# Kernel optimization log

Measured on AMD Instinct MI355X. Metric: run time of the kernel, lower is better.

## Reference

```python
import jax, jax.numpy as jnp
import numpy as np
import math

H = 12          # num_attention_heads
DIM = 768       # hidden_size
HD = DIM // H   # attention_head_size
B = 8           # batch
S = 1024        # max_seqlen
NNZ = B * S     # total_nnz (all sequences full length)


def setup_inputs() -> dict:
    key = jax.random.key(0)
    k1, k2, k3, k4 = jax.random.split(key, 4)
    hidden_states = jax.random.normal(k1, (NNZ, DIM), jnp.float32)
    cu_seqlens = jnp.arange(B + 1, dtype=jnp.int32) * S
    indices = jnp.arange(NNZ, dtype=jnp.int32)
    attn_mask = jnp.ones((B, S), jnp.int32)
    bias = jax.random.normal(k2, (B, H, S, S), jnp.float32) * 0.1
    slopes = jax.random.uniform(k3, (H,), jnp.float32)
    # Wqkv = nn.Linear(DIM, 3*DIM): weight (3*DIM, DIM), bias (3*DIM,)
    Wqkv_w = jax.random.normal(k4, (3 * DIM, DIM), jnp.float32) * (1.0 / math.sqrt(DIM))
    Wqkv_b = jnp.zeros((3 * DIM,), jnp.float32)
    return {
        "hidden_states": hidden_states,
        "cu_seqlens": cu_seqlens,
        "max_seqlen": S,
        "indices": indices,
        "attn_mask": attn_mask,
        "bias": bias,
        "slopes": slopes,
        "Wqkv_w": Wqkv_w,
        "Wqkv_b": Wqkv_b,
    }


def reference(hidden_states, cu_seqlens, max_seqlen, indices, attn_mask, bias, slopes, Wqkv_w, Wqkv_b):
    nnz, dim = hidden_states.shape
    batch = cu_seqlens.shape[0] - 1
    hd = dim // H
    # fused QKV projection on unpadded tokens
    qkv = hidden_states @ Wqkv_w.T + Wqkv_b                      # (nnz, 3*dim)
    # pad_input: scatter tokens into dense (batch*seqlen, 3*dim)
    padded = jnp.zeros((batch * max_seqlen, 3 * dim), qkv.dtype).at[indices].set(qkv)
    qkv = padded.reshape(batch, max_seqlen, 3, H, hd)            # (b, s, 3, h, d)
    q, k, v = qkv[:, :, 0], qkv[:, :, 1], qkv[:, :, 2]           # (b, s, h, d)
    scores = jnp.einsum('bqhd,bkhd->bhqk', q, k) / math.sqrt(hd) + bias
    probs = jax.nn.softmax(scores, axis=-1)                      # (b, h, q, k)
    attn = jnp.einsum('bhqk,bkhd->bqhd', probs, v)               # (b, s, h, d)
    # unpad_input_only: gather valid tokens (attn_mask selects same positions as indices)
    flat = attn.reshape(batch * max_seqlen, dim)
    return flat[indices].reshape(nnz, dim)
```

## Files before the change

### kernel.cpp

```cpp
#include <hip/hip_runtime.h>

#define H_      12
#define DIM_    768
#define HD_     64
#define BATCH_  8
#define SEQ_    1024
#define NNZ_    8192
#define N3_     2304

typedef short sh8 __attribute__((ext_vector_type(8)));
typedef float f32x4 __attribute__((ext_vector_type(4)));

__device__ __forceinline__ unsigned short f2bf(float f) {
    unsigned u = __float_as_uint(f);
    u += 0x7fff + ((u >> 16) & 1);
    return (unsigned short)(u >> 16);
}

__device__ __forceinline__ void glds16(const unsigned short* g, unsigned short* l) {
    __builtin_amdgcn_global_load_lds(
        (const __attribute__((address_space(1))) unsigned int*)g,
        (__attribute__((address_space(3))) unsigned int*)l, 16, 0, 0);
}

__global__ void prep(const float* __restrict__ hidden,
                     const float* __restrict__ W,
                     const int* __restrict__ indices,
                     unsigned short* __restrict__ Xbf,
                     unsigned short* __restrict__ Wbf,
                     int* __restrict__ inv) {
    const int XN4 = NNZ_ * DIM_ / 4;
    const int WN4 = N3_ * DIM_ / 4;
    int i = blockIdx.x * blockDim.x + threadIdx.x;
    if (i < XN4) {
        float4 f = ((const float4*)hidden)[i];
        ushort4 u;
        u.x = f2bf(f.x); u.y = f2bf(f.y); u.z = f2bf(f.z); u.w = f2bf(f.w);
        ((ushort4*)Xbf)[i] = u;
    } else if (i < XN4 + WN4) {
        int k = i - XN4;
        float4 f = ((const float4*)W)[k];
        ushort4 u;
        u.x = f2bf(f.x); u.y = f2bf(f.y); u.z = f2bf(f.z); u.w = f2bf(f.w);
        ((ushort4*)Wbf)[k] = u;
    }
    if (i < NNZ_) inv[indices[i]] = i;
}

#define BK 32
__launch_bounds__(256)
__global__ void qkv_gemm(const unsigned short* __restrict__ X,
                         const unsigned short* __restrict__ W,
                         const float* __restrict__ bqkv,
                         const int* __restrict__ indices,
                         unsigned short* __restrict__ qkvbf) {
    __shared__ __align__(16) unsigned short As[2][128 * BK];
    __shared__ __align__(16) unsigned short Bs[2][128 * BK];

    const int orig = blockIdx.y * gridDim.x + blockIdx.x;
    const int c = orig & 7;
    const int local = orig >> 3;
    const int bm = ((c & 3) * 16 + (local & 15)) * 128;
    const int bn = ((c >> 2) * 9 + (local >> 4)) * 128;

    const int t = threadIdx.x;
    const int wave = t >> 6;
    const int lane = t & 63;
    const int l16 = lane & 15;
    const int quad = lane >> 4;
    const int wm = (wave & 1) * 64;
    const int wn = (wave >> 1) * 64;
    const int qxr = quad ^ ((l16 >> 1) & 3);

    f32x4 acc[4][4];
    for (int i = 0; i < 4; i++)
        for (int j = 0; j < 4; j++)
            for (int r = 0; r < 4; r++) acc[i][j][r] = 0.f;

    const int c0 = wave * 2;
    const int r0 = c0 * 16 + (lane >> 2);
    const int sslot = ((lane & 3) ^ ((lane >> 3) & 3)) * 8;
    const unsigned short* gA0 = &X[(size_t)(bm + r0) * DIM_ + sslot];
    const unsigned short* gA1 = &X[(size_t)(bm + r0 + 16) * DIM_ + sslot];
    const unsigned short* gB0 = &W[(size_t)(bn + r0) * DIM_ + sslot];
    const unsigned short* gB1 = &W[(size_t)(bn + r0 + 16) * DIM_ + sslot];
    unsigned short* lA0[2] = { &As[0][c0 * 512], &As[1][c0 * 512] };
    unsigned short* lB0[2] = { &Bs[0][c0 * 512], &Bs[1][c0 * 512] };

    glds16(gA0, lA0[0]);
    glds16(gA1, lA0[0] + 512);
    glds16(gB0, lB0[0]);
    glds16(gB1, lB0[0] + 512);
    __syncthreads();

    for (int ks = 0; ks < DIM_ / BK; ks++) {
        const int cur = ks & 1;

        if (ks < DIM_ / BK - 1) {
            const int kk = (ks + 1) * BK;
            if (cur == 0) {
                glds16(gA0 + kk, lA0[1]);
                glds16(gA1 + kk, lA0[1] + 512);
                glds16(gB0 + kk, lB0[1]);
                glds16(gB1 + kk, lB0[1] + 512);
            } else {
                glds16(gA0 + kk, lA0[0]);
                glds16(gA1 + kk, lA0[0] + 512);
                glds16(gB0 + kk, lB0[0]);
                glds16(gB1 + kk, lB0[0] + 512);
            }
        }
        __builtin_amdgcn_sched_barrier(0);

        sh8 af[4], wf[4];
        for (int i = 0; i < 4; i++)
            af[i] = *(const sh8*)&As[cur][(wm + i * 16 + l16) * BK + qxr * 8];
        for (int j = 0; j < 4; j++)
            wf[j] = *(const sh8*)&Bs[cur][(wn + j * 16 + l16) * BK + qxr * 8];
        for (int i = 0; i < 4; i++)
            for (int j = 0; j < 4; j++)
                acc[i][j] = __builtin_amdgcn_mfma_f32_16x16x32_bf16(af[i], wf[j], acc[i][j], 0, 0, 0);

        __syncthreads();
    }

    const size_t plane = (size_t)BATCH_ * H_ * SEQ_ * HD_;
    for (int i = 0; i < 4; i++) {
        for (int r = 0; r < 4; r++) {
            int m = bm + wm + i * 16 + quad * 4 + r;
            int pos = indices[m];
            int b = pos >> 10;
            int s = pos & 1023;
            for (int j = 0; j < 4; j++) {
                int n = bn + wn + j * 16 + l16;
                float val = acc[i][j][r] + bqkv[n];
                int which = n / DIM_;
                int nn = n - which * DIM_;
                int hh = nn >> 6;
                int d = nn & 63;
                size_t off;
                if (which == 2)
                    off = 2 * plane + (((size_t)b * H_ + hh) * HD_ + d) * SEQ_ + s;
                else
                    off = (size_t)which * plane + (((size_t)b * H_ + hh) * SEQ_ + s) * HD_ + d;
                qkvbf[off] = f2bf(val);
            }
        }
    }
}

#define LDP 72
__launch_bounds__(256, 3)
__global__ void attn(const unsigned short* __restrict__ qkvbf,
                     const float* __restrict__ bias,
                     const int* __restrict__ inv,
                     float* __restrict__ out) {
    __shared__ __align__(16) unsigned short Kp[2][2][64 * 32];
    __shared__ __align__(16) unsigned short Vp[2][2][64 * 32];
    __shared__ __align__(16) unsigned short Ps[4][16 * LDP];

    const int orig = blockIdx.y * gridDim.x + blockIdx.x;
    const int swz = (orig & 7) * 192 + (orig >> 3);
    const int qt = swz & 15;
    const int bh = swz >> 4;

    const int t = threadIdx.x;
    const int wave = t >> 6;
    const int lane = t & 63;
    const int l16 = lane & 15;
    const int quad = lane >> 4;
    const int qx = quad ^ ((l16 >> 1) & 3);

    const size_t plane = (size_t)BATCH_ * H_ * SEQ_ * HD_;
    const unsigned short* Q  = qkvbf + (size_t)bh * SEQ_ * HD_;
    const unsigned short* K  = Q + plane;
    const unsigned short* Vt = qkvbf + 2 * plane + (size_t)bh * HD_ * SEQ_;

    const int q0 = qt * 64 + wave * 16;

    sh8 aq[2];
    for (int kk2 = 0; kk2 < 2; kk2++)
        aq[kk2] = *(const sh8*)&Q[(size_t)(q0 + l16) * HD_ + kk2 * 32 + quad * 8];

    float lsum = 0.f;
    f32x4 o[4];
    for (int j = 0; j < 4; j++)
        for (int r = 0; r < 4; r++) o[j][r] = 0.f;

    const float scale = 0.125f;
    const float* brow4 = bias + (size_t)bh * SEQ_ * SEQ_ + (size_t)(q0 + l16) * SEQ_ + quad * 4;

    const int lrow = wave * 16 + (lane >> 2);
    const int lslot = (lane & 3) ^ ((lane >> 3) & 3);
    const unsigned short* gK = &K[(size_t)lrow * HD_ + lslot * 8];
    const unsigned short* gV = &Vt[(size_t)lrow * SEQ_ + lslot * 8];
    unsigned short* lK0[2] = { &Kp[0][0][wave * 512], &Kp[0][1][wave * 512] };
    unsigned short* lK1[2] = { &Kp[1][0][wave * 512], &Kp[1][1][wave * 512] };
    unsigned short* lV0[2] = { &Vp[0][0][wave * 512], &Vp[0][1][wave * 512] };
    unsigned short* lV1[2] = { &Vp[1][0][wave * 512], &Vp[1][1][wave * 512] };

    glds16(gK,      lK0[0]);
    glds16(gK + 32, lK0[1]);
    glds16(gV,      lV0[0]);
    glds16(gV + 32, lV0[1]);
    float4 bv4[4];
    for (int j = 0; j < 4; j++)
        bv4[j] = *(const float4*)(brow4 + j * 16);
    __syncthreads();

    for (int kt = 0; kt < 16; kt++) {
        const int cur = kt & 1;

        if (kt < 15) {
            const int k0n = (kt + 1) * 64;
            if (cur == 0) {
                glds16(gK + (size_t)k0n * HD_,      lK1[0]);
                glds16(gK + (size_t)k0n * HD_ + 32, lK1[1]);
                glds16(gV + k0n,      lV1[0]);
                glds16(gV + k0n + 32, lV1[1]);
            } else {
                glds16(gK + (size_t)k0n * HD_,      lK0[0]);
                glds16(gK + (size_t)k0n * HD_ + 32, lK0[1]);
                glds16(gV + k0n,      lV0[0]);
                glds16(gV + k0n + 32, lV0[1]);
            }
        }
        float4 bvn[4];
        {
            const int kb = ((kt + 1) & 15) * 64;
            for (int j = 0; j < 4; j++)
                bvn[j] = *(const float4*)(brow4 + kb + j * 16);
        }
        __builtin_amdgcn_sched_barrier(0);

        f32x4 sc[4];
        for (int j = 0; j < 4; j++)
            for (int r = 0; r < 4; r++) sc[j][r] = 0.f;
        for (int kk2 = 0; kk2 < 2; kk2++)
            for (int j = 0; j < 4; j++) {
                sh8 bk = *(const sh8*)&Kp[cur][kk2][(j * 16 + l16) * 32 + qx * 8];
                sc[j] = __builtin_amdgcn_mfma_f32_16x16x32_bf16(bk, aq[kk2], sc[j], 0, 0, 0);
            }

        for (int j = 0; j < 4; j++) {
            float4 bb = bv4[j];
            float p0 = __expf(sc[j][0] * scale + bb.x);
            float p1 = __expf(sc[j][1] * scale + bb.y);
            float p2 = __expf(sc[j][2] * scale + bb.z);
            float p3 = __expf(sc[j][3] * scale + bb.w);
            lsum += (p0 + p1) + (p2 + p3);
            ushort4 u;
            u.x = f2bf(p0); u.y = f2bf(p1); u.z = f2bf(p2); u.w = f2bf(p3);
            *(ushort4*)&Ps[wave][l16 * LDP + j * 16 + quad * 4] = u;
        }

        for (int kk2 = 0; kk2 < 2; kk2++) {
            sh8 ap = *(const sh8*)&Ps[wave][l16 * LDP + kk2 * 32 + quad * 8];
            for (int j = 0; j < 4; j++) {
                sh8 vvf = *(const sh8*)&Vp[cur][kk2][(j * 16 + l16) * 32 + qx * 8];
                o[j] = __builtin_amdgcn_mfma_f32_16x16x32_bf16(ap, vvf, o[j], 0, 0, 0);
            }
        }

        __syncthreads();
        for (int j = 0; j < 4; j++) bv4[j] = bvn[j];
    }

    float s0 = lsum;
    s0 += __shfl_xor(s0, 16, 64);
    s0 += __shfl_xor(s0, 32, 64);
    float rl[4];
    for (int r = 0; r < 4; r++)
        rl[r] = 1.0f / __shfl(s0, quad * 4 + r, 64);

    const int b = bh / H_;
    const int hh = bh % H_;
    for (int r = 0; r < 4; r++) {
        int srow_q = q0 + quad * 4 + r;
        int pos = b * SEQ_ + srow_q;
        int i_out = inv[pos];
        for (int j = 0; j < 4; j++)
            out[(size_t)i_out * DIM_ + hh * HD_ + j * 16 + l16] = o[j][r] * rl[r];
    }
}

extern "C" void kernel_launch(void* const* d_in, const int* in_sizes, int n_in,
                              void* d_out, int out_size, void* d_ws, size_t ws_size,
                              hipStream_t stream) {
    const float* hidden  = (const float*)d_in[0];
    const int*   indices = (const int*)d_in[3];
    const float* bias    = (const float*)d_in[5];
    const float* Wqkv_w  = (const float*)d_in[7];
    const float* Wqkv_b  = (const float*)d_in[8];
    float* out = (float*)d_out;

    char* ws = (char*)d_ws;
    unsigned short* Xbf   = (unsigned short*)ws;
    unsigned short* Wbf   = (unsigned short*)(ws + 12582912);
    unsigned short* qkvbf = (unsigned short*)(ws + 16121856);
    int* inv              = (int*)(ws + 53870592);

    const int XN4 = NNZ_ * DIM_ / 4;
    const int WN4 = N3_ * DIM_ / 4;
    prep<<<(XN4 + WN4 + 255) / 256, 256, 0, stream>>>(hidden, Wqkv_w, indices, Xbf, Wbf, inv);
    qkv_gemm<<<dim3(NNZ_ / 128, N3_ / 128), 256, 0, stream>>>(Xbf, Wbf, Wqkv_b, indices, qkvbf);
    attn<<<dim3(SEQ_ / 64, BATCH_ * H_), 256, 0, stream>>>(qkvbf, bias, inv, out);
}
```

Baseline: 625.3 us.

## Double attention query tile to 128 rows with 8 waves sharing K/V loads

The attention kernel now uses 512 threads (8 waves) per block and covers 128 query rows, so each K/V tile staged in LDS serves twice as many queries and the grid is halved. Each wave now loads half as many K/V bytes into LDS. The bias register prefetch for the next tile is removed, and bias is loaded at the top of each iteration instead, which lowers register use but may expose global load latency. Launch bounds change to 512 threads with a minimum of 4 blocks.

```diff
diff --git a/kernel.cpp b/kernel.cpp
--- a/kernel.cpp
+++ b/kernel.cpp
@@ -150,19 +150,19 @@
 }
 
 #define LDP 72
-__launch_bounds__(256, 3)
+__launch_bounds__(512, 4)
 __global__ void attn(const unsigned short* __restrict__ qkvbf,
                      const float* __restrict__ bias,
                      const int* __restrict__ inv,
                      float* __restrict__ out) {
     __shared__ __align__(16) unsigned short Kp[2][2][64 * 32];
     __shared__ __align__(16) unsigned short Vp[2][2][64 * 32];
-    __shared__ __align__(16) unsigned short Ps[4][16 * LDP];
+    __shared__ __align__(16) unsigned short Ps[8][16 * LDP];
 
     const int orig = blockIdx.y * gridDim.x + blockIdx.x;
-    const int swz = (orig & 7) * 192 + (orig >> 3);
-    const int qt = swz & 15;
-    const int bh = swz >> 4;
+    const int swz = (orig & 7) * 96 + (orig >> 3);
+    const int qt = swz & 7;
+    const int bh = swz >> 3;
 
     const int t = threadIdx.x;
     const int wave = t >> 6;
@@ -176,7 +176,7 @@
     const unsigned short* K  = Q + plane;
     const unsigned short* Vt = qkvbf + 2 * plane + (size_t)bh * HD_ * SEQ_;
 
-    const int q0 = qt * 64 + wave * 16;
+    const int q0 = qt * 128 + wave * 16;
 
     sh8 aq[2];
     for (int kk2 = 0; kk2 < 2; kk2++)
@@ -190,47 +190,35 @@
     const float scale = 0.125f;
     const float* brow4 = bias + (size_t)bh * SEQ_ * SEQ_ + (size_t)(q0 + l16) * SEQ_ + quad * 4;
 
-    const int lrow = wave * 16 + (lane >> 2);
+    const int hHalf = wave & 1;
+    const int rBase = (wave >> 1) * 16;
     const int lslot = (lane & 3) ^ ((lane >> 3) & 3);
-    const unsigned short* gK = &K[(size_t)lrow * HD_ + lslot * 8];
-    const unsigned short* gV = &Vt[(size_t)lrow * SEQ_ + lslot * 8];
-    unsigned short* lK0[2] = { &Kp[0][0][wave * 512], &Kp[0][1][wave * 512] };
-    unsigned short* lK1[2] = { &Kp[1][0][wave * 512], &Kp[1][1][wave * 512] };
-    unsigned short* lV0[2] = { &Vp[0][0][wave * 512], &Vp[0][1][wave * 512] };
-    unsigned short* lV1[2] = { &Vp[1][0][wave * 512], &Vp[1][1][wave * 512] };
-
-    glds16(gK,      lK0[0]);
-    glds16(gK + 32, lK0[1]);
-    glds16(gV,      lV0[0]);
-    glds16(gV + 32, lV0[1]);
-    float4 bv4[4];
-    for (int j = 0; j < 4; j++)
-        bv4[j] = *(const float4*)(brow4 + j * 16);
+    const unsigned short* gK = &K[(size_t)(rBase + (lane >> 2)) * HD_ + hHalf * 32 + lslot * 8];
+    const unsigned short* gV = &Vt[(size_t)(rBase + (lane >> 2)) * SEQ_ + hHalf * 32 + lslot * 8];
+    unsigned short* lKd[2] = { &Kp[0][hHalf][rBase * 32], &Kp[1][hHalf][rBase * 32] };
+    unsigned short* lVd[2] = { &Vp[0][hHalf][rBase * 32], &Vp[1][hHalf][rBase * 32] };
+
+    glds16(gK, lKd[0]);
+    glds16(gV, lVd[0]);
     __syncthreads();
 
     for (int kt = 0; kt < 16; kt++) {
         const int cur = kt & 1;
+        const int k0 = kt * 64;
 
         if (kt < 15) {
-            const int k0n = (kt + 1) * 64;
+            const int k0n = k0 + 64;
             if (cur == 0) {
-                glds16(gK + (size_t)k0n * HD_,      lK1[0]);
-                glds16(gK + (size_t)k0n * HD_ + 32, lK1[1]);
-                glds16(gV + k0n,      lV1[0]);
-                glds16(gV + k0n + 32, lV1[1]);
+                glds16(gK + (size_t)k0n * HD_, lKd[1]);
+                glds16(gV + k0n,               lVd[1]);
             } else {
-                glds16(gK + (size_t)k0n * HD_,      lK0[0]);
-                glds16(gK + (size_t)k0n * HD_ + 32, lK0[1]);
-                glds16(gV + k0n,      lV0[0]);
-                glds16(gV + k0n + 32, lV0[1]);
-            }
-        }
-        float4 bvn[4];
-        {
-            const int kb = ((kt + 1) & 15) * 64;
-            for (int j = 0; j < 4; j++)
-                bvn[j] = *(const float4*)(brow4 + kb + j * 16);
-        }
+                glds16(gK + (size_t)k0n * HD_, lKd[0]);
+                glds16(gV + k0n,               lVd[0]);
+            }
+        }
+        float4 bv[4];
+        for (int j = 0; j < 4; j++)
+            bv[j] = *(const float4*)(brow4 + k0 + j * 16);
         __builtin_amdgcn_sched_barrier(0);
 
         f32x4 sc[4];
@@ -243,7 +231,7 @@
             }
 
         for (int j = 0; j < 4; j++) {
-            float4 bb = bv4[j];
+            float4 bb = bv[j];
             float p0 = __expf(sc[j][0] * scale + bb.x);
             float p1 = __expf(sc[j][1] * scale + bb.y);
             float p2 = __expf(sc[j][2] * scale + bb.z);
@@ -263,7 +251,6 @@
         }
 
         __syncthreads();
-        for (int j = 0; j < 4; j++) bv4[j] = bvn[j];
     }
 
     float s0 = lsum;
@@ -304,5 +291,5 @@
     const int WN4 = N3_ * DIM_ / 4;
     prep<<<(XN4 + WN4 + 255) / 256, 256, 0, stream>>>(hidden, Wqkv_w, indices, Xbf, Wbf, inv);
     qkv_gemm<<<dim3(NNZ_ / 128, N3_ / 128), 256, 0, stream>>>(Xbf, Wbf, Wqkv_b, indices, qkvbf);
-    attn<<<dim3(SEQ_ / 64, BATCH_ * H_), 256, 0, stream>>>(qkvbf, bias, inv, out);
-}
+    attn<<<dim3(SEQ_ / 128, BATCH_ * H_), 512, 0, stream>>>(qkvbf, bias, inv, out);
+}
```

New measurement: 645.3 us. 3.2% more time.
